# Kernel tuning notes

Measured on AMD Instinct MI355X. Metric: run time of the kernel, lower is better.

The kernel has to match this reference:

```python
import jax, jax.numpy as jnp
import numpy as np

V, E, H, ENC, ATT, S = 32000, 512, 1024, 1024, 512, 128
B, L, T = 64, 64, 15
BOS = 1

def setup_inputs():
    key = jax.random.key(0)
    ks = jax.random.split(key, 16)
    g = lambda k, shape, scale=0.02: jax.random.normal(k, shape, jnp.float32) * scale
    return {
        "enc_output": jax.random.normal(ks[0], (B, L, ENC), jnp.float32),
        "enc_len": jax.random.randint(ks[1], (B,), 1, L + 1),
        "styles": jax.random.randint(ks[2], (B,), 0, 2),
        "emb_table": g(ks[3], (V, E)),
        "style_table": g(ks[4], (2, S), 1.0),
        "Wq": g(ks[5], (ATT, H)), "bq": jnp.zeros((ATT,), jnp.float32),
        "Wk": g(ks[6], (ATT, ENC)),
        "Wc": g(ks[7], (ATT,)),          # mlp_coverage: Linear(1, att), no bias
        "Wo": g(ks[8], (ATT,)),          # mlp_out: Linear(att, 1), no bias
        "W_ih": g(ks[9], (3 * H, E + S + ENC)), "b_ih": jnp.zeros((3 * H,), jnp.float32),
        "W_hh": g(ks[10], (3 * H, H)), "b_hh": jnp.zeros((3 * H,), jnp.float32),
        "W1": g(ks[11], (H, ENC + H)), "b1": jnp.zeros((H,), jnp.float32),
        "W2": g(ks[12], (V, H)), "b2": jnp.zeros((V,), jnp.float32),
    }

def gru_cell(x, h, W_ih, b_ih, W_hh, b_hh):
    gi = x @ W_ih.T + b_ih
    gh = h @ W_hh.T + b_hh
    i_r, i_z, i_n = jnp.split(gi, 3, axis=-1)
    h_r, h_z, h_n = jnp.split(gh, 3, axis=-1)
    r = jax.nn.sigmoid(i_r + h_r)
    z = jax.nn.sigmoid(i_z + h_z)
    n = jnp.tanh(i_n + r * h_n)
    return (1.0 - z) * n + z * h

def reference(enc_output, enc_len, styles, emb_table, style_table, Wq, bq, Wk, Wc, Wo,
              W_ih, b_ih, W_hh, b_hh, W1, b1, W2, b2):
    style_emb = style_table[styles]                                  # [B, S]
    keys_proj = jnp.einsum('bld,ad->bla', enc_output, Wk)            # hoisted: same every step
    pad_mask = jnp.arange(L)[None, :] >= enc_len[:, None]            # [B, L], True = padded

    def step(carry, _):
        h, ctx, cov, prev = carry
        emb = emb_table[prev]                                        # [B, E]
        x = jnp.concatenate([emb, style_emb, ctx], axis=-1)          # [B, E+S+ENC]
        h = gru_cell(x, h, W_ih, b_ih, W_hh, b_hh)                   # [B, H]
        # additive coverage attention
        q = h @ Wq.T + bq                                            # [B, ATT]
        cov_proj = cov[:, :, None] * Wc[None, None, :]               # [B, L, ATT]
        energy = jnp.tanh(q[:, None, :] + keys_proj + cov_proj) @ Wo  # [B, L]
        energy = jnp.where(pad_mask, -1e10, energy)
        attn = jax.nn.softmax(energy, axis=-1)                       # [B, L]
        ctx = jnp.einsum('bl,bld->bd', attn, enc_output)             # [B, ENC]
        o = jnp.concatenate([ctx, h], axis=-1) @ W1.T + b1
        o = jnp.where(o >= 0, o, 0.1 * o)                            # LeakyReLU(0.1)
        logit = o @ W2.T + b2                                        # [B, V]
        pred = jnp.argmax(logit, axis=-1)
        return (h, ctx, cov + attn, pred), (logit, attn, pred)

    h0 = jnp.zeros((B, H), enc_output.dtype)
    c0 = jnp.zeros((B, ENC), enc_output.dtype)
    cov0 = jnp.zeros((B, L), enc_output.dtype)
    bos = jnp.full((B,), BOS, jnp.int32)
    _, (logits, attns, preds) = jax.lax.scan(step, (h0, c0, cov0, bos), None, length=T)
    logits = jnp.transpose(logits, (1, 0, 2))                        # [B, T, V]
    attns = jnp.transpose(attns, (1, 0, 2))                          # [B, T, L]
    preds = jnp.transpose(preds, (1, 0))                             # [B, T]
    log_probs = jax.nn.log_softmax(logits, axis=-1)
    dec_log_probs = jnp.take_along_axis(log_probs, preds[:, :, None], axis=2)[:, :, 0]
    return logits, dec_log_probs, preds, attns
```

## Files before the change

### kernel.cpp

```cpp
#include <hip/hip_runtime.h>
#include <hip/hip_bf16.h>
#include <stdint.h>
#include <stddef.h>

#define B_    64
#define L_    64
#define T_    15
#define V_    32000
#define E_    512
#define H_    1024
#define ENC_  1024
#define ATT_  512
#define S_    128

#define DEC_OFF  30720000
#define PRED_OFF 30720960
#define ATT_OFF  30721920

template<int AMODE, int OUTMODE, int NT>
__global__ __launch_bounds__(256) void gemm_b(
    const float* __restrict__ W, int N, int K, int KB,
    const float* __restrict__ AT,
    const float* __restrict__ Af,
    const float* __restrict__ stab,
    const int* __restrict__ previ,
    const int* __restrict__ styles,
    const float* __restrict__ chT,
    const float* __restrict__ bias,
    float* __restrict__ Cout, size_t zstride, int c_sn, int c_sm,
    float* __restrict__ out2, int t,
    float* __restrict__ pmax, float* __restrict__ psum, int* __restrict__ pidx)
{
  constexpr int JT  = NT / 4;
  constexpr int WLD = NT / 32;
  __shared__ float Ws[NT * 36];
  const int tid  = threadIdx.x;
  const int lane = tid & 63;
  const int wv   = tid >> 6;
  const int n0   = blockIdx.x * NT;
  const int m0   = blockIdx.y * 64;
  const int kb0  = blockIdx.z * KB;

  long erow = 0, srow = 0;
  if (AMODE == 1) {
    int pv = previ[lane];
    if (pv < 0 || pv >= V_) pv = 0;
    erow = (long)pv * E_;
    srow = (long)styles[lane] * S_;
  }

  auto xfetch = [&](int k) -> float {
    if (k < E_)            return Af[erow + k];
    else if (k < E_ + S_)  return stab[srow + (k - E_)];
    else                   return chT[(size_t)(k - (E_ + S_)) * 64 + lane];
  };

  auto ldW = [&](int kc, float4* u) {
    if constexpr (NT == 64) {
      int n = tid >> 2, k8 = (tid & 3) * 8;
      const float4* wp = (const float4*)(W + (size_t)(n0 + n) * K + kc + k8);
      u[0] = wp[0]; u[1] = wp[1];
    } else {
      int n = tid >> 3, k4 = (tid & 7) * 4;
      const float4* wp = (const float4*)(W + (size_t)(n0 + n) * K + kc + k4);
      u[0] = wp[0];
    }
  };
  auto stW = [&](const float4* u) {
    if constexpr (NT == 64) {
      int n = tid >> 2, k8 = (tid & 3) * 8;
      float* ds = &Ws[n * 36 + k8];
      ds[0] = u[0].x; ds[1] = u[0].y; ds[2] = u[0].z; ds[3] = u[0].w;
      ds[4] = u[1].x; ds[5] = u[1].y; ds[6] = u[1].z; ds[7] = u[1].w;
    } else {
      int n = tid >> 3, k4 = (tid & 7) * 4;
      float* ds = &Ws[n * 36 + k4];
      ds[0] = u[0].x; ds[1] = u[0].y; ds[2] = u[0].z; ds[3] = u[0].w;
    }
  };

  float acc[JT];
#pragma unroll
  for (int j = 0; j < JT; ++j) acc[j] = 0.f;

  float4 cu[WLD], nu[WLD];
  ldW(kb0, cu);

  for (int kc = kb0; kc < kb0 + KB; kc += 32) {
    stW(cu);
    __syncthreads();

    float a[32];
    if constexpr (AMODE == 0) {
#pragma unroll
      for (int kk = 0; kk < 32; ++kk)
        a[kk] = AT[(size_t)(kc + kk) * 64 + lane];
    } else if constexpr (AMODE == 2) {
      const float4* ar = (const float4*)(Af + (size_t)(m0 + lane) * K + kc);
#pragma unroll
      for (int kk = 0; kk < 8; ++kk) {
        float4 u = ar[kk];
        a[4 * kk] = u.x; a[4 * kk + 1] = u.y; a[4 * kk + 2] = u.z; a[4 * kk + 3] = u.w;
      }
    } else {
#pragma unroll
      for (int kk = 0; kk < 32; ++kk) a[kk] = xfetch(kc + kk);
    }

    if (kc + 32 < kb0 + KB) ldW(kc + 32, nu);

    const float* wr0 = &Ws[(wv * JT) * 36];
#pragma unroll
    for (int k = 0; k < 32; k += 4) {
#pragma unroll
      for (int j = 0; j < JT; ++j) {
        float4 w = *(const float4*)(wr0 + j * 36 + k);
        acc[j] = fmaf(w.x, a[k + 0], acc[j]);
        acc[j] = fmaf(w.y, a[k + 1], acc[j]);
        acc[j] = fmaf(w.z, a[k + 2], acc[j]);
        acc[j] = fmaf(w.w, a[k + 3], acc[j]);
      }
    }
    __syncthreads();
#pragma unroll
    for (int i = 0; i < WLD; ++i) cu[i] = nu[i];
  }

  const int nbase = n0 + wv * JT;
  if (OUTMODE == 0) {
    float* cb = Cout + (size_t)blockIdx.z * zstride;
#pragma unroll
    for (int j = 0; j < JT; ++j) {
      float c = acc[j];
      if (bias) c += bias[nbase + j];
      cb[(size_t)(nbase + j) * c_sn + (size_t)(m0 + lane) * c_sm] = c;
    }
  } else {
    float vmax = -__builtin_inff(); float s = 0.f; int vidx = 0x7fffffff;
    float ob[JT];
#pragma unroll
    for (int j = 0; j < JT; ++j) {
      float c = acc[j] + bias[nbase + j];
      ob[j] = c;
      if (c > vmax) { s = s * __expf(vmax - c) + 1.f; vmax = c; vidx = nbase + j; }
      else          { s += __expf(c - vmax); }
    }
    float* op = out2 + (size_t)lane * (T_ * V_) + (size_t)t * V_ + nbase;
#pragma unroll
    for (int jq = 0; jq < JT / 4; ++jq) {
      float4 q;
      q.x = ob[4 * jq + 0]; q.y = ob[4 * jq + 1];
      q.z = ob[4 * jq + 2]; q.w = ob[4 * jq + 3];
      ((float4*)op)[jq] = q;
    }
    int pb = (blockIdx.x * 4 + wv) * 64 + lane;
    pmax[pb] = vmax; psum[pb] = s; pidx[pb] = vidx;
  }
}

__global__ __launch_bounds__(256) void gru_combine(
    const float* __restrict__ gip, const float* __restrict__ ghp,
    const float* __restrict__ b_ih, const float* __restrict__ b_hh,
    float* __restrict__ chT)
{
  int tgl = blockIdx.x * 256 + threadIdx.x;
  int b = tgl & 63; int i = tgl >> 6;
  float ir = b_ih[i], iz = b_ih[H_ + i], in_ = b_ih[2 * H_ + i];
  float hr = b_hh[i], hz = b_hh[H_ + i], hn  = b_hh[2 * H_ + i];
  for (int kz = 0; kz < 13; ++kz) {
    const float* p = gip + (size_t)kz * (3 * H_ * 64);
    ir  += p[(size_t)i * 64 + b];
    iz  += p[(size_t)(H_ + i) * 64 + b];
    in_ += p[(size_t)(2 * H_ + i) * 64 + b];
  }
  for (int kz = 0; kz < 8; ++kz) {
    const float* p = ghp + (size_t)kz * (3 * H_ * 64);
    hr += p[(size_t)i * 64 + b];
    hz += p[(size_t)(H_ + i) * 64 + b];
    hn += p[(size_t)(2 * H_ + i) * 64 + b];
  }
  float r = 1.f / (1.f + expf(-(ir + hr)));
  float z = 1.f / (1.f + expf(-(iz + hz)));
  float n = tanhf(in_ + r * hn);
  float h = chT[(size_t)(H_ + i) * 64 + b];
  chT[(size_t)(H_ + i) * 64 + b] = (1.f - z) * n + z * h;
}

__global__ __launch_bounds__(256) void o_combine(
    const float* __restrict__ op, const float* __restrict__ b1,
    float* __restrict__ oT)
{
  int tgl = blockIdx.x * 256 + threadIdx.x;
  int b = tgl & 63; int i = tgl >> 6;
  float v = b1[i];
  for (int kz = 0; kz < 8; ++kz) v += op[(size_t)kz * (H_ * 64) + (size_t)i * 64 + b];
  v = (v >= 0.f) ? v : 0.1f * v;
  oT[(size_t)i * 64 + b] = v;
}

__global__ __launch_bounds__(256) void energy_kernel(
    const float* __restrict__ qp,
    const float* __restrict__ kp,
    const float* __restrict__ cov,
    const float* __restrict__ Wc, const float* __restrict__ Wo,
    const float* __restrict__ bq,
    const int* __restrict__ enc_len,
    float* __restrict__ en)
{
  const int lane = threadIdx.x & 63;
  const int wv   = threadIdx.x >> 6;
  const int w    = blockIdx.x * 4 + wv;
  const int b    = w >> 6;
  const int l    = w & 63;

  const float cv = cov[b * L_ + l];
  const float* kpr = kp + ((size_t)b * L_ + l) * ATT_;
  const float* qb  = qp + (size_t)b * ATT_;

  float e = 0.f;
#pragma unroll
  for (int i = 0; i < 8; ++i) {
    int a = lane + i * 64;
    float q = bq[a];
#pragma unroll
    for (int z = 0; z < 8; ++z) q += qb[(size_t)z * (B_ * ATT_) + a];
    e += tanhf(q + kpr[a] + cv * Wc[a]) * Wo[a];
  }
#pragma unroll
  for (int off = 32; off > 0; off >>= 1) e += __shfl_down(e, off);
  if (lane == 0) en[b * L_ + l] = (l < enc_len[b]) ? e : -1e10f;
}

__global__ __launch_bounds__(256) void softmax_ctx(
    const float* __restrict__ en,
    float* __restrict__ cov,
    float* __restrict__ out_attn,
    const float* __restrict__ enc,
    float* __restrict__ chT, int t)
{
  __shared__ float a_s[L_];
  const int b     = blockIdx.x >> 2;
  const int chunk = blockIdx.x & 3;
  const int tid   = threadIdx.x;

  if (tid < L_) {
    float v = en[b * L_ + tid];
    float mx = v;
#pragma unroll
    for (int off = 32; off > 0; off >>= 1) mx = fmaxf(mx, __shfl_xor(mx, off));
    float ex = expf(v - mx);
    float sm = ex;
#pragma unroll
    for (int off = 32; off > 0; off >>= 1) sm += __shfl_xor(sm, off);
    float at = ex / sm;
    a_s[tid] = at;
    if (chunk == 0) {
      cov[b * L_ + tid] += at;
      out_attn[((size_t)b * T_ + t) * L_ + tid] = at;
    }
  }
  __syncthreads();

  const int d = chunk * 256 + tid;
  const float* ep = enc + ((size_t)b * L_) * ENC_ + d;
  float acc0 = 0.f, acc1 = 0.f, acc2 = 0.f, acc3 = 0.f;
#pragma unroll
  for (int l = 0; l < L_; l += 4) {
    acc0 = fmaf(a_s[l + 0], ep[(size_t)(l + 0) * ENC_], acc0);
    acc1 = fmaf(a_s[l + 1], ep[(size_t)(l + 1) * ENC_], acc1);
    acc2 = fmaf(a_s[l + 2], ep[(size_t)(l + 2) * ENC_], acc2);
    acc3 = fmaf(a_s[l + 3], ep[(size_t)(l + 3) * ENC_], acc3);
  }
  chT[(size_t)d * 64 + b] = acc0 + acc1 + acc2 + acc3;
}

__global__ __launch_bounds__(256) void lse_final(
    const float* __restrict__ pmax, const float* __restrict__ psum,
    const int* __restrict__ pidx,
    float* __restrict__ out, int* __restrict__ previ, int t, int NP)
{
  __shared__ float smx[4]; __shared__ int sid[4]; __shared__ float ssm[4];
  int b = blockIdx.x; int tid = threadIdx.x;
  int lane = tid & 63; int wv = tid >> 6;

  float vmax = -__builtin_inff(); int vidx = 0x7fffffff;
  for (int p = tid; p < NP; p += 256) {
    float v = pmax[(size_t)p * 64 + b]; int i = pidx[(size_t)p * 64 + b];
    if (v > vmax || (v == vmax && i < vidx)) { vmax = v; vidx = i; }
  }
#pragma unroll
  for (int off = 32; off > 0; off >>= 1) {
    float ov = __shfl_xor(vmax, off); int oi = __shfl_xor(vidx, off);
    if (ov > vmax || (ov == vmax && oi < vidx)) { vmax = ov; vidx = oi; }
  }
  if (lane == 0) { smx[wv] = vmax; sid[wv] = vidx; }
  __syncthreads();
  float gmax = smx[0]; int gidx = sid[0];
#pragma unroll
  for (int w = 1; w < 4; ++w) {
    float v = smx[w]; int i = sid[w];
    if (v > gmax || (v == gmax && i < gidx)) { gmax = v; gidx = i; }
  }

  float s = 0.f;
  for (int p = tid; p < NP; p += 256)
    s += psum[(size_t)p * 64 + b] * __expf(pmax[(size_t)p * 64 + b] - gmax);
#pragma unroll
  for (int off = 32; off > 0; off >>= 1) s += __shfl_xor(s, off);
  if (lane == 0) ssm[wv] = s;
  __syncthreads();
  if (tid == 0) {
    s = ssm[0] + ssm[1] + ssm[2] + ssm[3];
    if (gidx < 0 || gidx >= V_) gidx = 0;
    out[DEC_OFF  + b * T_ + t] = -logf(s);
    out[PRED_OFF + b * T_ + t] = (float)gidx;
    previ[b] = gidx;
  }
}

__global__ __launch_bounds__(256) void init_state(float* chT, float* cov, int* previ)
{
  int tgl = blockIdx.x * 256 + threadIdx.x;
  if (tgl < 2048 * 64) chT[tgl] = 0.f;
  else if (tgl < 2048 * 64 + 64 * 64) cov[tgl - 2048 * 64] = 0.f;
  else if (tgl < 2048 * 64 + 64 * 64 + 64) previ[tgl - (2048 * 64 + 64 * 64)] = 1;
}

extern "C" void kernel_launch(void* const* d_in, const int* in_sizes, int n_in,
                              void* d_out, int out_size, void* d_ws, size_t ws_size,
                              hipStream_t stream)
{
  const float* enc     = (const float*)d_in[0];
  const int*   enc_len = (const int*)d_in[1];
  const int*   styles  = (const int*)d_in[2];
  const float* emb     = (const float*)d_in[3];
  const float* stab    = (const float*)d_in[4];
  const float* Wq      = (const float*)d_in[5];
  const float* bq      = (const float*)d_in[6];
  const float* Wk      = (const float*)d_in[7];
  const float* Wc      = (const float*)d_in[8];
  const float* Wo      = (const float*)d_in[9];
  const float* W_ih    = (const float*)d_in[10];
  const float* b_ih    = (const float*)d_in[11];
  const float* W_hh    = (const float*)d_in[12];
  const float* b_hh    = (const float*)d_in[13];
  const float* W1      = (const float*)d_in[14];
  const float* b1      = (const float*)d_in[15];
  const float* W2      = (const float*)d_in[16];
  const float* b2      = (const float*)d_in[17];
  float* out = (float*)d_out;

  char* ws = (char*)d_ws;
  float* kp   = (float*)(ws + 0);
  float* chT  = (float*)(ws + 8388608);
  float* cov  = (float*)(ws + 8912896);
  float* gi_p = (float*)(ws + 8929280);
  float* gh_p = (float*)(ws + 19152896);
  float* o_p  = (float*)(ws + 25444352);
  float* oT   = (float*)(ws + 27541504);
  int*   prev = (int*)  (ws + 29339648);

  float* qp   = gi_p;
  float* en   = gi_p + 8 * B_ * ATT_;

  float* pmax = gh_p;
  float* psum = gh_p + 4000 * 64;
  int*   pidx = (int*)(gh_p + 2 * 4000 * 64);

  init_state<<<529, 256, 0, stream>>>(chT, cov, prev);

  gemm_b<2, 0, 64><<<dim3(8, 64, 1), 256, 0, stream>>>(
      Wk, ATT_, ENC_, ENC_,
      nullptr, enc, nullptr, nullptr, nullptr, nullptr, nullptr,
      kp, 0, 1, ATT_, nullptr, 0, nullptr, nullptr, nullptr);

  for (int t = 0; t < T_; ++t) {
    gemm_b<1, 0, 32><<<dim3(96, 1, 13), 256, 0, stream>>>(
        W_ih, 3 * H_, 1664, 128,
        nullptr, emb, stab, prev, styles, chT, nullptr,
        gi_p, (size_t)3 * H_ * 64, 64, 1, nullptr, 0, nullptr, nullptr, nullptr);
    gemm_b<0, 0, 32><<<dim3(96, 1, 8), 256, 0, stream>>>(
        W_hh, 3 * H_, H_, 128,
        chT + (size_t)H_ * 64, nullptr, nullptr, nullptr, nullptr, nullptr, nullptr,
        gh_p, (size_t)3 * H_ * 64, 64, 1, nullptr, 0, nullptr, nullptr, nullptr);
    gru_combine<<<256, 256, 0, stream>>>(gi_p, gh_p, b_ih, b_hh, chT);

    gemm_b<0, 0, 32><<<dim3(16, 1, 8), 256, 0, stream>>>(
        Wq, ATT_, H_, 128,
        chT + (size_t)H_ * 64, nullptr, nullptr, nullptr, nullptr, nullptr, nullptr,
        qp, (size_t)B_ * ATT_, 1, ATT_,
        nullptr, 0, nullptr, nullptr, nullptr);
    energy_kernel<<<1024, 256, 0, stream>>>(qp, kp, cov, Wc, Wo, bq, enc_len, en);
    softmax_ctx<<<256, 256, 0, stream>>>(en, cov, out + ATT_OFF, enc, chT, t);

    gemm_b<0, 0, 32><<<dim3(32, 1, 8), 256, 0, stream>>>(
        W1, H_, 2 * H_, 256,
        chT, nullptr, nullptr, nullptr, nullptr, nullptr, nullptr,
        o_p, (size_t)H_ * 64, 64, 1, nullptr, 0, nullptr, nullptr, nullptr);
    o_combine<<<256, 256, 0, stream>>>(o_p, b1, oT);
    gemm_b<0, 1, 32><<<dim3(1000, 1, 1), 256, 0, stream>>>(
        W2, V_, H_, H_,
        oT, nullptr, nullptr, nullptr, nullptr, nullptr, b2,
        nullptr, 0, 0, 0, out, t, pmax, psum, pidx);
    lse_final<<<64, 256, 0, stream>>>(pmax, psum, pidx, out, prev, t, 4000);
  }
}
```

Baseline: 4.184 ms.

## Read weight rows directly from global memory per wave instead of staging in LDS

The GEMM kernel no longer stages weight tiles through shared memory with block-wide barriers. Each wave now owns JT output rows and reads them straight from global memory as wave-uniform float4 loads, while the activation column is double-buffered in registers. Several launches are reshaped (more blocks with fewer rows per wave) to keep occupancy up. This removes the LDS round trip and the two barriers per k-chunk. In exchange it relies on scalar or broadcast global loads and caches for the weight stream.

```diff
diff --git a/kernel.cpp b/kernel.cpp
--- a/kernel.cpp
+++ b/kernel.cpp
@@ -17,9 +17,9 @@
 #define PRED_OFF 30720960
 #define ATT_OFF  30721920
 
-template<int AMODE, int OUTMODE, int NT>
-__global__ __launch_bounds__(256) void gemm_b(
-    const float* __restrict__ W, int N, int K, int KB,
+template<int AMODE, int OUTMODE, int JT>
+__global__ __launch_bounds__(256) void gemm_s(
+    const float* __restrict__ W, int K, int KB,
     const float* __restrict__ AT,
     const float* __restrict__ Af,
     const float* __restrict__ stab,
@@ -31,13 +31,11 @@
     float* __restrict__ out2, int t,
     float* __restrict__ pmax, float* __restrict__ psum, int* __restrict__ pidx)
 {
-  constexpr int JT  = NT / 4;
-  constexpr int WLD = NT / 32;
-  __shared__ float Ws[NT * 36];
   const int tid  = threadIdx.x;
   const int lane = tid & 63;
-  const int wv   = tid >> 6;
-  const int n0   = blockIdx.x * NT;
+  const int wv   = __builtin_amdgcn_readfirstlane(tid >> 6);
+  const int wid  = blockIdx.x * 4 + wv;
+  const int n0   = wid * JT;
   const int m0   = blockIdx.y * 64;
   const int kb0  = blockIdx.z * KB;
 
@@ -55,42 +53,7 @@
     else                   return chT[(size_t)(k - (E_ + S_)) * 64 + lane];
   };
 
-  auto ldW = [&](int kc, float4* u) {
-    if constexpr (NT == 64) {
-      int n = tid >> 2, k8 = (tid & 3) * 8;
-      const float4* wp = (const float4*)(W + (size_t)(n0 + n) * K + kc + k8);
-      u[0] = wp[0]; u[1] = wp[1];
-    } else {
-      int n = tid >> 3, k4 = (tid & 7) * 4;
-      const float4* wp = (const float4*)(W + (size_t)(n0 + n) * K + kc + k4);
-      u[0] = wp[0];
-    }
-  };
-  auto stW = [&](const float4* u) {
-    if constexpr (NT == 64) {
-      int n = tid >> 2, k8 = (tid & 3) * 8;
-      float* ds = &Ws[n * 36 + k8];
-      ds[0] = u[0].x; ds[1] = u[0].y; ds[2] = u[0].z; ds[3] = u[0].w;
-      ds[4] = u[1].x; ds[5] = u[1].y; ds[6] = u[1].z; ds[7] = u[1].w;
-    } else {
-      int n = tid >> 3, k4 = (tid & 7) * 4;
-      float* ds = &Ws[n * 36 + k4];
-      ds[0] = u[0].x; ds[1] = u[0].y; ds[2] = u[0].z; ds[3] = u[0].w;
-    }
-  };
-
-  float acc[JT];
-#pragma unroll
-  for (int j = 0; j < JT; ++j) acc[j] = 0.f;
-
-  float4 cu[WLD], nu[WLD];
-  ldW(kb0, cu);
-
-  for (int kc = kb0; kc < kb0 + KB; kc += 32) {
-    stW(cu);
-    __syncthreads();
-
-    float a[32];
+  auto loadA = [&](int kc, float* a) {
     if constexpr (AMODE == 0) {
 #pragma unroll
       for (int kk = 0; kk < 32; ++kk)
@@ -100,52 +63,63 @@
 #pragma unroll
       for (int kk = 0; kk < 8; ++kk) {
         float4 u = ar[kk];
-        a[4 * kk] = u.x; a[4 * kk + 1] = u.y; a[4 * kk + 2] = u.z; a[4 * kk + 3] = u.w;
+        a[4 * kk + 0] = u.x; a[4 * kk + 1] = u.y;
+        a[4 * kk + 2] = u.z; a[4 * kk + 3] = u.w;
       }
     } else {
 #pragma unroll
       for (int kk = 0; kk < 32; ++kk) a[kk] = xfetch(kc + kk);
     }
-
-    if (kc + 32 < kb0 + KB) ldW(kc + 32, nu);
-
-    const float* wr0 = &Ws[(wv * JT) * 36];
-#pragma unroll
-    for (int k = 0; k < 32; k += 4) {
-#pragma unroll
-      for (int j = 0; j < JT; ++j) {
-        float4 w = *(const float4*)(wr0 + j * 36 + k);
-        acc[j] = fmaf(w.x, a[k + 0], acc[j]);
-        acc[j] = fmaf(w.y, a[k + 1], acc[j]);
-        acc[j] = fmaf(w.z, a[k + 2], acc[j]);
-        acc[j] = fmaf(w.w, a[k + 3], acc[j]);
+  };
+
+  float acc[JT];
+#pragma unroll
+  for (int j = 0; j < JT; ++j) acc[j] = 0.f;
+
+  auto rowsFMA = [&](int kc, const float* a) {
+    const float* wp = W + (size_t)n0 * K + kc;
+#pragma unroll
+    for (int j = 0; j < JT; ++j) {
+      const float4* wr = (const float4*)(wp + (size_t)j * K);
+#pragma unroll
+      for (int k4 = 0; k4 < 8; ++k4) {
+        float4 w = wr[k4];
+        acc[j] = fmaf(w.x, a[4 * k4 + 0], acc[j]);
+        acc[j] = fmaf(w.y, a[4 * k4 + 1], acc[j]);
+        acc[j] = fmaf(w.z, a[4 * k4 + 2], acc[j]);
+        acc[j] = fmaf(w.w, a[4 * k4 + 3], acc[j]);
       }
     }
-    __syncthreads();
-#pragma unroll
-    for (int i = 0; i < WLD; ++i) cu[i] = nu[i];
-  }
-
-  const int nbase = n0 + wv * JT;
+  };
+
+  float aA[32], aB[32];
+  loadA(kb0, aA);
+  for (int kc = kb0; kc < kb0 + KB; kc += 64) {
+    loadA(kc + 32, aB);
+    rowsFMA(kc, aA);
+    if (kc + 64 < kb0 + KB) loadA(kc + 64, aA);
+    rowsFMA(kc + 32, aB);
+  }
+
   if (OUTMODE == 0) {
     float* cb = Cout + (size_t)blockIdx.z * zstride;
 #pragma unroll
     for (int j = 0; j < JT; ++j) {
       float c = acc[j];
-      if (bias) c += bias[nbase + j];
-      cb[(size_t)(nbase + j) * c_sn + (size_t)(m0 + lane) * c_sm] = c;
+      if (bias) c += bias[n0 + j];
+      cb[(size_t)(n0 + j) * c_sn + (size_t)(m0 + lane) * c_sm] = c;
     }
   } else {
     float vmax = -__builtin_inff(); float s = 0.f; int vidx = 0x7fffffff;
     float ob[JT];
 #pragma unroll
     for (int j = 0; j < JT; ++j) {
-      float c = acc[j] + bias[nbase + j];
+      float c = acc[j] + bias[n0 + j];
       ob[j] = c;
-      if (c > vmax) { s = s * __expf(vmax - c) + 1.f; vmax = c; vidx = nbase + j; }
+      if (c > vmax) { s = s * __expf(vmax - c) + 1.f; vmax = c; vidx = n0 + j; }
       else          { s += __expf(c - vmax); }
     }
-    float* op = out2 + (size_t)lane * (T_ * V_) + (size_t)t * V_ + nbase;
+    float* op = out2 + (size_t)lane * (T_ * V_) + (size_t)t * V_ + n0;
 #pragma unroll
     for (int jq = 0; jq < JT / 4; ++jq) {
       float4 q;
@@ -153,7 +127,7 @@
       q.z = ob[4 * jq + 2]; q.w = ob[4 * jq + 3];
       ((float4*)op)[jq] = q;
     }
-    int pb = (blockIdx.x * 4 + wv) * 64 + lane;
+    int pb = wid * 64 + lane;
     pmax[pb] = vmax; psum[pb] = s; pidx[pb] = vidx;
   }
 }
@@ -369,37 +343,37 @@
 
   init_state<<<529, 256, 0, stream>>>(chT, cov, prev);
 
-  gemm_b<2, 0, 64><<<dim3(8, 64, 1), 256, 0, stream>>>(
-      Wk, ATT_, ENC_, ENC_,
+  gemm_s<2, 0, 8><<<dim3(16, 64, 1), 256, 0, stream>>>(
+      Wk, ENC_, ENC_,
       nullptr, enc, nullptr, nullptr, nullptr, nullptr, nullptr,
       kp, 0, 1, ATT_, nullptr, 0, nullptr, nullptr, nullptr);
 
   for (int t = 0; t < T_; ++t) {
-    gemm_b<1, 0, 32><<<dim3(96, 1, 13), 256, 0, stream>>>(
-        W_ih, 3 * H_, 1664, 128,
+    gemm_s<1, 0, 8><<<dim3(96, 1, 13), 256, 0, stream>>>(
+        W_ih, 1664, 128,
         nullptr, emb, stab, prev, styles, chT, nullptr,
         gi_p, (size_t)3 * H_ * 64, 64, 1, nullptr, 0, nullptr, nullptr, nullptr);
-    gemm_b<0, 0, 32><<<dim3(96, 1, 8), 256, 0, stream>>>(
-        W_hh, 3 * H_, H_, 128,
+    gemm_s<0, 0, 4><<<dim3(192, 1, 8), 256, 0, stream>>>(
+        W_hh, H_, 128,
         chT + (size_t)H_ * 64, nullptr, nullptr, nullptr, nullptr, nullptr, nullptr,
         gh_p, (size_t)3 * H_ * 64, 64, 1, nullptr, 0, nullptr, nullptr, nullptr);
     gru_combine<<<256, 256, 0, stream>>>(gi_p, gh_p, b_ih, b_hh, chT);
 
-    gemm_b<0, 0, 32><<<dim3(16, 1, 8), 256, 0, stream>>>(
-        Wq, ATT_, H_, 128,
+    gemm_s<0, 0, 4><<<dim3(32, 1, 8), 256, 0, stream>>>(
+        Wq, H_, 128,
         chT + (size_t)H_ * 64, nullptr, nullptr, nullptr, nullptr, nullptr, nullptr,
         qp, (size_t)B_ * ATT_, 1, ATT_,
         nullptr, 0, nullptr, nullptr, nullptr);
     energy_kernel<<<1024, 256, 0, stream>>>(qp, kp, cov, Wc, Wo, bq, enc_len, en);
     softmax_ctx<<<256, 256, 0, stream>>>(en, cov, out + ATT_OFF, enc, chT, t);
 
-    gemm_b<0, 0, 32><<<dim3(32, 1, 8), 256, 0, stream>>>(
-        W1, H_, 2 * H_, 256,
+    gemm_s<0, 0, 4><<<dim3(64, 1, 8), 256, 0, stream>>>(
+        W1, 2 * H_, 256,
         chT, nullptr, nullptr, nullptr, nullptr, nullptr, nullptr,
         o_p, (size_t)H_ * 64, 64, 1, nullptr, 0, nullptr, nullptr, nullptr);
     o_combine<<<256, 256, 0, stream>>>(o_p, b1, oT);
-    gemm_b<0, 1, 32><<<dim3(1000, 1, 1), 256, 0, stream>>>(
-        W2, V_, H_, H_,
+    gemm_s<0, 1, 8><<<dim3(1000, 1, 1), 256, 0, stream>>>(
+        W2, H_, H_,
         oT, nullptr, nullptr, nullptr, nullptr, nullptr, b2,
         nullptr, 0, 0, 0, out, t, pmax, psum, pidx);
     lse_final<<<64, 256, 0, stream>>>(pmax, psum, pidx, out, prev, t, 4000);
```

Result: slower. 7.436 ms (+77.7%).

## Add register-blocked double-buffered logits GEMM with fused partial argmax/LSE

Applied to the files above, without the earlier changes.

Replaces the generic W2 logits GEMM with a dedicated kernel. Each block computes a 64x64 tile and each thread holds a 4x4 register tile, so shared-memory loads are reused across both vocab and batch. The kernel double-buffers the global-to-LDS staging of W2 and activations, and merges partial max/sum/argmax across lanes with shuffles. This halves the number of partial entries lse_final must reduce. The vocab projection is the largest GEMM per step, and the aim is higher arithmetic intensity per LDS load and overlap of global loads with compute. The cost is more register pressure and fewer blocks (500).

```diff
diff --git a/kernel.cpp b/kernel.cpp
--- a/kernel.cpp
+++ b/kernel.cpp
@@ -17,7 +17,7 @@
 #define PRED_OFF 30720960
 #define ATT_OFF  30721920
 
-template<int AMODE, int OUTMODE, int NT>
+template<int AMODE, int NT>
 __global__ __launch_bounds__(256) void gemm_b(
     const float* __restrict__ W, int N, int K, int KB,
     const float* __restrict__ AT,
@@ -27,9 +27,7 @@
     const int* __restrict__ styles,
     const float* __restrict__ chT,
     const float* __restrict__ bias,
-    float* __restrict__ Cout, size_t zstride, int c_sn, int c_sm,
-    float* __restrict__ out2, int t,
-    float* __restrict__ pmax, float* __restrict__ psum, int* __restrict__ pidx)
+    float* __restrict__ Cout, size_t zstride, int c_sn, int c_sm)
 {
   constexpr int JT  = NT / 4;
   constexpr int WLD = NT / 32;
@@ -127,34 +125,134 @@
   }
 
   const int nbase = n0 + wv * JT;
-  if (OUTMODE == 0) {
-    float* cb = Cout + (size_t)blockIdx.z * zstride;
-#pragma unroll
-    for (int j = 0; j < JT; ++j) {
-      float c = acc[j];
-      if (bias) c += bias[nbase + j];
-      cb[(size_t)(nbase + j) * c_sn + (size_t)(m0 + lane) * c_sm] = c;
-    }
-  } else {
+  float* cb = Cout + (size_t)blockIdx.z * zstride;
+#pragma unroll
+  for (int j = 0; j < JT; ++j) {
+    float c = acc[j];
+    if (bias) c += bias[nbase + j];
+    cb[(size_t)(nbase + j) * c_sn + (size_t)(m0 + lane) * c_sm] = c;
+  }
+}
+
+__global__ __launch_bounds__(256) void logits_kernel(
+    const float* __restrict__ W2, const float* __restrict__ oT,
+    const float* __restrict__ b2,
+    float* __restrict__ out2, int t,
+    float* __restrict__ pmax, float* __restrict__ psum, int* __restrict__ pidx)
+{
+  __shared__ float Ws[2][64 * 36];
+  __shared__ float As[2][32 * 64];
+  const int tid  = threadIdx.x;
+  const int lane = tid & 63;
+  const int wv   = tid >> 6;
+  const int q    = lane >> 4;
+  const int m4   = (lane & 15) * 4;
+  const int n0   = blockIdx.x * 64;
+  const int nb   = n0 + wv * 16 + q * 4;
+
+  const int sr = tid >> 2;
+  const int sk = (tid & 3) * 8;
+
+  float4 wr0, wr1, ar0, ar1;
+  auto ldG = [&](int kc) {
+    const float4* wp = (const float4*)(W2 + (size_t)(n0 + sr) * H_ + kc + sk);
+    wr0 = wp[0]; wr1 = wp[1];
+    const float4* ap = (const float4*)(oT + (size_t)kc * 64);
+    ar0 = ap[tid]; ar1 = ap[256 + tid];
+  };
+  auto stg = [&](int buf) {
+    float* wd = &Ws[buf][sr * 36 + sk];
+    wd[0] = wr0.x; wd[1] = wr0.y; wd[2] = wr0.z; wd[3] = wr0.w;
+    wd[4] = wr1.x; wd[5] = wr1.y; wd[6] = wr1.z; wd[7] = wr1.w;
+    float4* ad = (float4*)As[buf];
+    ad[tid] = ar0; ad[256 + tid] = ar1;
+  };
+
+  float4 acc[4];
+#pragma unroll
+  for (int j = 0; j < 4; ++j) acc[j] = make_float4(0.f, 0.f, 0.f, 0.f);
+
+  ldG(0); stg(0);
+  __syncthreads();
+
+  for (int it = 0; it < 32; ++it) {
+    const int cur = it & 1;
+    if (it < 31) ldG((it + 1) * 32);
+
+    const float* wbase = &Ws[cur][(wv * 16 + q * 4) * 36];
+    const float* abase = As[cur];
+#pragma unroll
+    for (int ks = 0; ks < 32; ks += 8) {
+      float4 af[8];
+#pragma unroll
+      for (int kk = 0; kk < 8; ++kk)
+        af[kk] = *(const float4*)(abase + (ks + kk) * 64 + m4);
+#pragma unroll
+      for (int j = 0; j < 4; ++j) {
+        const float* wp = wbase + j * 36 + ks;
+        float4 w0 = *(const float4*)(wp);
+        float4 w1 = *(const float4*)(wp + 4);
+#define FMA4(wv_, a_) \
+        acc[j].x = fmaf(wv_, a_.x, acc[j].x); \
+        acc[j].y = fmaf(wv_, a_.y, acc[j].y); \
+        acc[j].z = fmaf(wv_, a_.z, acc[j].z); \
+        acc[j].w = fmaf(wv_, a_.w, acc[j].w);
+        FMA4(w0.x, af[0]) FMA4(w0.y, af[1]) FMA4(w0.z, af[2]) FMA4(w0.w, af[3])
+        FMA4(w1.x, af[4]) FMA4(w1.y, af[5]) FMA4(w1.z, af[6]) FMA4(w1.w, af[7])
+#undef FMA4
+      }
+    }
+    if (it < 31) stg(cur ^ 1);
+    __syncthreads();
+  }
+
+  float cj[4][4];
+#pragma unroll
+  for (int j = 0; j < 4; ++j) {
+    float bj = b2[nb + j];
+    cj[j][0] = acc[j].x + bj; cj[j][1] = acc[j].y + bj;
+    cj[j][2] = acc[j].z + bj; cj[j][3] = acc[j].w + bj;
+  }
+
+#pragma unroll
+  for (int mi = 0; mi < 4; ++mi) {
+    float4 v = make_float4(cj[0][mi], cj[1][mi], cj[2][mi], cj[3][mi]);
+    *(float4*)(out2 + (size_t)(m4 + mi) * (T_ * V_) + (size_t)t * V_ + nb) = v;
+  }
+
+  float vm[4], ss[4]; int vi[4];
+#pragma unroll
+  for (int mi = 0; mi < 4; ++mi) {
     float vmax = -__builtin_inff(); float s = 0.f; int vidx = 0x7fffffff;
-    float ob[JT];
-#pragma unroll
-    for (int j = 0; j < JT; ++j) {
-      float c = acc[j] + bias[nbase + j];
-      ob[j] = c;
-      if (c > vmax) { s = s * __expf(vmax - c) + 1.f; vmax = c; vidx = nbase + j; }
+#pragma unroll
+    for (int j = 0; j < 4; ++j) {
+      float c = cj[j][mi];
+      if (c > vmax) { s = s * __expf(vmax - c) + 1.f; vmax = c; vidx = nb + j; }
       else          { s += __expf(c - vmax); }
     }
-    float* op = out2 + (size_t)lane * (T_ * V_) + (size_t)t * V_ + nbase;
-#pragma unroll
-    for (int jq = 0; jq < JT / 4; ++jq) {
-      float4 q;
-      q.x = ob[4 * jq + 0]; q.y = ob[4 * jq + 1];
-      q.z = ob[4 * jq + 2]; q.w = ob[4 * jq + 3];
-      ((float4*)op)[jq] = q;
-    }
-    int pb = (blockIdx.x * 4 + wv) * 64 + lane;
-    pmax[pb] = vmax; psum[pb] = s; pidx[pb] = vidx;
+    vm[mi] = vmax; ss[mi] = s; vi[mi] = vidx;
+  }
+#pragma unroll
+  for (int off = 16; off <= 32; off <<= 1) {
+#pragma unroll
+    for (int mi = 0; mi < 4; ++mi) {
+      float om = __shfl_xor(vm[mi], off);
+      float os = __shfl_xor(ss[mi], off);
+      int   oi = __shfl_xor(vi[mi], off);
+      float nm = fmaxf(vm[mi], om);
+      ss[mi] = ss[mi] * __expf(vm[mi] - nm) + os * __expf(om - nm);
+      vi[mi] = (om > vm[mi] || (om == vm[mi] && oi < vi[mi])) ? oi : vi[mi];
+      vm[mi] = nm;
+    }
+  }
+  if (q == 0) {
+    int pb = blockIdx.x * 4 + wv;
+#pragma unroll
+    for (int mi = 0; mi < 4; ++mi) {
+      pmax[(size_t)pb * 64 + m4 + mi] = vm[mi];
+      psum[(size_t)pb * 64 + m4 + mi] = ss[mi];
+      pidx[(size_t)pb * 64 + m4 + mi] = vi[mi];
+    }
   }
 }
 
@@ -364,44 +462,41 @@
   float* en   = gi_p + 8 * B_ * ATT_;
 
   float* pmax = gh_p;
-  float* psum = gh_p + 4000 * 64;
-  int*   pidx = (int*)(gh_p + 2 * 4000 * 64);
+  float* psum = gh_p + 2000 * 64;
+  int*   pidx = (int*)(gh_p + 2 * 2000 * 64);
 
   init_state<<<529, 256, 0, stream>>>(chT, cov, prev);
 
-  gemm_b<2, 0, 64><<<dim3(8, 64, 1), 256, 0, stream>>>(
+  gemm_b<2, 64><<<dim3(8, 64, 1), 256, 0, stream>>>(
       Wk, ATT_, ENC_, ENC_,
       nullptr, enc, nullptr, nullptr, nullptr, nullptr, nullptr,
-      kp, 0, 1, ATT_, nullptr, 0, nullptr, nullptr, nullptr);
+      kp, 0, 1, ATT_);
 
   for (int t = 0; t < T_; ++t) {
-    gemm_b<1, 0, 32><<<dim3(96, 1, 13), 256, 0, stream>>>(
+    gemm_b<1, 32><<<dim3(96, 1, 13), 256, 0, stream>>>(
         W_ih, 3 * H_, 1664, 128,
         nullptr, emb, stab, prev, styles, chT, nullptr,
-        gi_p, (size_t)3 * H_ * 64, 64, 1, nullptr, 0, nullptr, nullptr, nullptr);
-    gemm_b<0, 0, 32><<<dim3(96, 1, 8), 256, 0, stream>>>(
+        gi_p, (size_t)3 * H_ * 64, 64, 1);
+    gemm_b<0, 32><<<dim3(96, 1, 8), 256, 0, stream>>>(
         W_hh, 3 * H_, H_, 128,
         chT + (size_t)H_ * 64, nullptr, nullptr, nullptr, nullptr, nullptr, nullptr,
-        gh_p, (size_t)3 * H_ * 64, 64, 1, nullptr, 0, nullptr, nullptr, nullptr);
+        gh_p, (size_t)3 * H_ * 64, 64, 1);
     gru_combine<<<256, 256, 0, stream>>>(gi_p, gh_p, b_ih, b_hh, chT);
 
-    gemm_b<0, 0, 32><<<dim3(16, 1, 8), 256, 0, stream>>>(
+    gemm_b<0, 32><<<dim3(16, 1, 8), 256, 0, stream>>>(
         Wq, ATT_, H_, 128,
         chT + (size_t)H_ * 64, nullptr, nullptr, nullptr, nullptr, nullptr, nullptr,
-        qp, (size_t)B_ * ATT_, 1, ATT_,
-        nullptr, 0, nullptr, nullptr, nullptr);
+        qp, (size_t)B_ * ATT_, 1, ATT_);
     energy_kernel<<<1024, 256, 0, stream>>>(qp, kp, cov, Wc, Wo, bq, enc_len, en);
     softmax_ctx<<<256, 256, 0, stream>>>(en, cov, out + ATT_OFF, enc, chT, t);
 
-    gemm_b<0, 0, 32><<<dim3(32, 1, 8), 256, 0, stream>>>(
+    gemm_b<0, 32><<<dim3(32, 1, 8), 256, 0, stream>>>(
         W1, H_, 2 * H_, 256,
         chT, nullptr, nullptr, nullptr, nullptr, nullptr, nullptr,
-        o_p, (size_t)H_ * 64, 64, 1, nullptr, 0, nullptr, nullptr, nullptr);
+        o_p, (size_t)H_ * 64, 64, 1);
     o_combine<<<256, 256, 0, stream>>>(o_p, b1, oT);
-    gemm_b<0, 1, 32><<<dim3(1000, 1, 1), 256, 0, stream>>>(
-        W2, V_, H_, H_,
-        oT, nullptr, nullptr, nullptr, nullptr, nullptr, b2,
-        nullptr, 0, 0, 0, out, t, pmax, psum, pidx);
-    lse_final<<<64, 256, 0, stream>>>(pmax, psum, pidx, out, prev, t, 4000);
-  }
-}
+    logits_kernel<<<500, 256, 0, stream>>>(
+        W2, oT, b2, out, t, pmax, psum, pidx);
+    lse_final<<<64, 256, 0, stream>>>(pmax, psum, pidx, out, prev, t, 2000);
+  }
+}
```

After: 3.389 ms. 1.23x faster.
